# Optimization experiments

Hardware: AMD Instinct MI355X
Metric: run time of the kernel (lower is better)

The kernel has to match this reference:

```python
import jax, jax.numpy as jnp
import numpy as np

BN_EPS = 1e-5


def setup_inputs() -> dict:
    key = jax.random.key(0)
    ks = jax.random.split(key, 8)
    B, N, D = 16, 16384, 64
    NP, NS = 1024, 32
    inp = {
        "xyz": jax.random.normal(ks[0], (B, 3, N), dtype=jnp.float32),
        "points": jax.random.normal(ks[1], (B, D, N), dtype=jnp.float32),
        "fps_init": jax.random.randint(ks[2], (B,), 0, N, dtype=jnp.int32),
        "group_idx": jax.random.randint(ks[3], (B, NP, NS), 0, N, dtype=jnp.int32),
    }
    chans = [67, 64, 128, 128]
    for i in range(3):
        cin, cout = chans[i], chans[i + 1]
        wk = jax.random.fold_in(ks[4], i)
        inp[f"W{i}"] = jax.random.normal(wk, (cout, cin), dtype=jnp.float32) * (1.0 / np.sqrt(cin))
        inp[f"b{i}"] = jnp.zeros((cout,), dtype=jnp.float32)
        inp[f"g{i}"] = jnp.ones((cout,), dtype=jnp.float32)
        inp[f"be{i}"] = jnp.zeros((cout,), dtype=jnp.float32)
    return inp


def _fps(x, init_far, npoint):
    # x: [B,N,3]; iterative furthest point sampling, npoint sequential steps
    B, N, _ = x.shape

    def step(carry, _):
        dist, far = carry
        c = jnp.take_along_axis(x, far[:, None, None], axis=1)  # [B,1,3]
        d = jnp.sum((x - c) ** 2, axis=-1)                       # [B,N]
        dist = jnp.minimum(dist, d)
        return (dist, jnp.argmax(dist, axis=-1).astype(far.dtype)), far

    init = (jnp.full((B, N), 1e10, dtype=x.dtype), init_far)
    _, cents = jax.lax.scan(step, init, None, length=npoint)
    return cents.T  # [B, npoint]


def _conv_bn_relu(h, W, b, g, be):
    # h: [B, np, ns, Cin]; 1x1 conv == channel matmul; BN (training stats) over (B,np,ns)
    y = jnp.einsum('bskc,oc->bsko', h, W) + b
    m = y.mean(axis=(0, 1, 2))
    v = y.var(axis=(0, 1, 2))
    y = (y - m) * jax.lax.rsqrt(v + BN_EPS) * g + be
    return jax.nn.relu(y)


def reference(xyz, points, fps_init, group_idx,
              W0, b0, g0, be0, W1, b1, g1, be1, W2, b2, g2, be2):
    x = jnp.transpose(xyz, (0, 2, 1))     # [B,N,3]
    p = jnp.transpose(points, (0, 2, 1))  # [B,N,D]
    B, N, _ = x.shape
    NP, NS = group_idx.shape[1], group_idx.shape[2]

    cents = _fps(x, fps_init, NP)                                   # [B,NP]
    new_xyz = jnp.take_along_axis(x, cents[:, :, None], axis=1)     # [B,NP,3]

    flat = group_idx.reshape(B, NP * NS)
    gx = jnp.take_along_axis(x, flat[:, :, None], axis=1).reshape(B, NP, NS, 3)
    gp = jnp.take_along_axis(p, flat[:, :, None], axis=1).reshape(B, NP, NS, -1)
    h = jnp.concatenate([gx, gp], axis=-1)  # [B,NP,NS,67]

    h = _conv_bn_relu(h, W0, b0, g0, be0)
    h = _conv_bn_relu(h, W1, b1, g1, be1)
    h = _conv_bn_relu(h, W2, b2, g2, be2)
    new_points = h.max(axis=2)              # max over nsample -> [B,NP,Cout]

    return jnp.transpose(new_xyz, (0, 2, 1)), jnp.transpose(new_points, (0, 2, 1))
```

## Files before the change

kernel.cpp:

```cpp
#include <hip/hip_runtime.h>

typedef short bf16x8 __attribute__((ext_vector_type(8)));
typedef float f32x4 __attribute__((ext_vector_type(4)));
typedef float f32x2 __attribute__((ext_vector_type(2)));
typedef unsigned short u16;
typedef unsigned int u32;
typedef unsigned long long u64;

#define NPTS 16384
#define NPOINT 1024
#define STOT 524288
#define NCB 240
#define NW  960

__device__ __forceinline__ u16 f2bf(float f){
  u32 u = __builtin_bit_cast(u32, f);
  u += 0x7fffu + ((u >> 16) & 1u);
  return (u16)(u >> 16);
}
__device__ __forceinline__ float bf2f(u16 u){
  u32 x = ((u32)u) << 16;
  return __builtin_bit_cast(float, x);
}

template<int CTRL>
__device__ __forceinline__ float dpp_maxf(float v){
  int x = __builtin_amdgcn_update_dpp(0, __builtin_bit_cast(int, v), CTRL, 0xf, 0xf, true);
  return fmaxf(v, __builtin_bit_cast(float, x));
}
template<int CTRL>
__device__ __forceinline__ u64 dpp_max(u64 key){
  u32 lo = (u32)key, hi = (u32)(key >> 32);
  u32 lo1 = (u32)__builtin_amdgcn_update_dpp(0, (int)lo, CTRL, 0xf, 0xf, true);
  u32 hi1 = (u32)__builtin_amdgcn_update_dpp(0, (int)hi, CTRL, 0xf, 0xf, true);
  u64 k1 = ((u64)hi1 << 32) | (u64)lo1;
  return (k1 > key) ? k1 : key;
}
__device__ __forceinline__ u64 packkey(float d, int idx){
  return ((u64)__builtin_bit_cast(u32, d) << 32) | (u64)(u32)(~(u32)idx);
}

__device__ __forceinline__ void arrive(u32* c){
  __hip_atomic_fetch_add(c, 1u, __ATOMIC_RELEASE, __HIP_MEMORY_SCOPE_AGENT);
}
__device__ __forceinline__ void waitc(u32* c, u32 tgt){
  while (__hip_atomic_load(c, __ATOMIC_ACQUIRE, __HIP_MEMORY_SCOPE_AGENT) < tgt)
    __builtin_amdgcn_s_sleep(16);
}

struct FpsS  { uint2 wkey[2][16]; float4 csl[2]; };
struct ConvS { float lsum[128]; float lsqr[128]; float av[128]; float dv[128]; };
union SMemU  { FpsS fps; ConvS conv; };

__device__ __forceinline__ bf16x8 load_bn_relu(const u16* __restrict__ row, int ko,
                                               const float* __restrict__ av,
                                               const float* __restrict__ dv){
  uint4 r = *(const uint4*)(row + ko);
  u32 w[4] = {r.x, r.y, r.z, r.w};
  bf16x8 out;
#pragma unroll
  for (int jj = 0; jj < 8; jj++){
    u16 us = (u16)(w[jj >> 1] >> ((jj & 1) * 16));
    float h = fmaxf(fmaf(av[ko + jj], bf2f(us), dv[ko + jj]), 0.f);
    out[jj] = (short)f2bf(h);
  }
  return out;
}

__global__ void zero_kernel(u32* __restrict__ ctrs){
  if (threadIdx.x < 64) ctrs[threadIdx.x] = 0;
}

__global__ __launch_bounds__(1024, 4) void mega_kernel(
    const float* __restrict__ xyz, const float* __restrict__ points,
    const int* __restrict__ finit, const int* __restrict__ gidx,
    const float* __restrict__ W0, const float* __restrict__ g0v, const float* __restrict__ be0,
    const float* __restrict__ W1, const float* __restrict__ g1v, const float* __restrict__ be1,
    const float* __restrict__ W2, const float* __restrict__ g2v, const float* __restrict__ be2,
    float* __restrict__ out0, float* __restrict__ out1,
    u16* __restrict__ XP, u16* __restrict__ y0, u16* __restrict__ y1,
    float* __restrict__ maxb, float* __restrict__ minb,
    float* __restrict__ statsF,
    u16* __restrict__ W0bf, u16* __restrict__ W1bf, u16* __restrict__ W2bf,
    u32* __restrict__ ctrs){
  __shared__ SMemU sm;
  const int t = threadIdx.x;
  const int wave = t >> 6, lane = t & 63;

  if (blockIdx.x < 16){
    const int b = blockIdx.x;
    const float* xb = xyz + (size_t)b * 3 * NPTS;
    f32x2 px[8], py[8], pz[8], dist[8];
#pragma unroll
    for (int j = 0; j < 8; j++){
      f32x2 x, y, z;
#pragma unroll
      for (int h = 0; h < 2; h++){
        int n = ((2*j + h) << 10) + t;
        x[h] = xb[n];
        y[h] = xb[NPTS + n];
        z[h] = xb[2*NPTS + n];
      }
      px[j] = x; py[j] = y; pz[j] = z;
      f32x2 big = {1e10f, 1e10f};
      dist[j] = big;
    }
    const int far0 = finit[b];
    if (t == (far0 & 1023)){
      int kk = far0 >> 10;
      float sx = px[0].x, sy = py[0].x, sz = pz[0].x;
#pragma unroll
      for (int k = 1; k < 16; k++){
        bool e = (kk == k);
        float vx = px[k>>1][k&1], vy = py[k>>1][k&1], vz = pz[k>>1][k&1];
        sx = e ? vx : sx; sy = e ? vy : sy; sz = e ? vz : sz;
      }
      sm.fps.csl[0] = make_float4(sx, sy, sz, 0.f);
    }
    __syncthreads();
    for (int it = 0; it < NPOINT; it++){
      const int p = it & 1;
      float4 cc = sm.fps.csl[p];
      if (t == 0){
        out0[((size_t)b*3 + 0)*NPOINT + it] = cc.x;
        out0[((size_t)b*3 + 1)*NPOINT + it] = cc.y;
        out0[((size_t)b*3 + 2)*NPOINT + it] = cc.z;
      }
      float bv = -1.f; int bk = 0;
      {
#pragma clang fp contract(off)
        f32x2 cx2 = {cc.x, cc.x}, cy2 = {cc.y, cc.y}, cz2 = {cc.z, cc.z};
#pragma unroll
        for (int j = 0; j < 8; j++){
          f32x2 dx = px[j] - cx2;
          f32x2 dy = py[j] - cy2;
          f32x2 dz = pz[j] - cz2;
          f32x2 dd = dx*dx + dy*dy + dz*dz;
          f32x2 dm = __builtin_elementwise_min(dist[j], dd);
          dist[j] = dm;
          bool g0 = dm.x > bv;
          bv = g0 ? dm.x : bv;  bk = g0 ? (2*j)   : bk;
          bool g1 = dm.y > bv;
          bv = g1 ? dm.y : bv;  bk = g1 ? (2*j+1) : bk;
        }
      }
      float m = bv;
      m = dpp_maxf<0xB1>(m);
      m = dpp_maxf<0x4E>(m);
      m = dpp_maxf<0x141>(m);
      m = dpp_maxf<0x140>(m);
      m = dpp_maxf<0x142>(m);
      m = dpp_maxf<0x143>(m);
      float ms = __builtin_bit_cast(float, __builtin_amdgcn_readlane(__builtin_bit_cast(int, m), 63));
      u64 mk = __ballot(bv == ms);
      u32 widx;
      if (__popcll(mk) == 1){
        int L = (int)__builtin_ctzll(mk);
        int kwin = __builtin_amdgcn_readlane(bk, L);
        widx = (u32)((kwin << 10) + (wave << 6) + L);
      } else {
        u64 key = packkey(bv, (bk << 10) + t);
        key = dpp_max<0xB1>(key); key = dpp_max<0x4E>(key);
        key = dpp_max<0x141>(key); key = dpp_max<0x140>(key);
        key = dpp_max<0x142>(key); key = dpp_max<0x143>(key);
        u32 lo = (u32)__builtin_amdgcn_readlane((int)(u32)key, 63);
        widx = ~lo;
      }
      if (lane == 0){
        uint2 wk; wk.x = widx; wk.y = __builtin_bit_cast(u32, ms);
        sm.fps.wkey[p][wave] = wk;
      }
      __syncthreads();
      uint2 wk = sm.fps.wkey[p][lane & 15];
      float wv = __builtin_bit_cast(float, wk.y);
      float g4 = wv;
      g4 = dpp_maxf<0xB1>(g4); g4 = dpp_maxf<0x4E>(g4);
      g4 = dpp_maxf<0x141>(g4); g4 = dpp_maxf<0x140>(g4);
      float gms = __builtin_bit_cast(float, __builtin_amdgcn_readfirstlane(__builtin_bit_cast(int, g4)));
      u64 mk2 = __ballot(wv == gms);
      u32 lo16 = (u32)mk2 & 0xFFFFu;
      int nb;
      if (__popc(lo16) == 1){
        int w = (int)__builtin_ctz(lo16);
        nb = __builtin_amdgcn_readlane((int)wk.x, w);
      } else {
        u64 k2 = ((u64)wk.y << 32) | (u64)(u32)(~wk.x);
        k2 = dpp_max<0xB1>(k2); k2 = dpp_max<0x4E>(k2);
        k2 = dpp_max<0x141>(k2); k2 = dpp_max<0x140>(k2);
        u32 lo = (u32)__builtin_amdgcn_readfirstlane((int)(u32)k2);
        nb = (int)~lo;
      }
      nb = __builtin_amdgcn_readfirstlane(nb);
      if (t == (nb & 1023)){
        int kk = nb >> 10;
        float sx = px[0].x, sy = py[0].x, sz = pz[0].x;
#pragma unroll
        for (int k = 1; k < 16; k++){
          bool e = (kk == k);
          float vx = px[k>>1][k&1], vy = py[k>>1][k&1], vz = pz[k>>1][k&1];
          sx = e ? vx : sx; sy = e ? vy : sy; sz = e ? vz : sz;
        }
        sm.fps.csl[p ^ 1] = make_float4(sx, sy, sz, 0.f);
      }
      __syncthreads();
    }
    return;
  }

  const int cb = blockIdx.x - 16;
  const int lw = wave & 3, g = wave >> 2;
  const int Wk = cb*4 + g;
  const int lrow = lane & 15, lq = lane >> 4;
  float* bsum0 = statsF;          float* bsqr0 = statsF + 8192;
  float* bsum1 = statsF + 16384;  float* bsqr1 = statsF + 24576;
  float* bsum2 = statsF + 32768;  float* bsqr2 = statsF + 40960;
  float* a0 = statsF + 49152;       float* d0 = a0 + 128;
  float* a1 = statsF + 49152 + 256; float* d1 = a1 + 128;
  float* a2 = statsF + 49152 + 512; float* d2 = a2 + 128;

  for (u32 idx = (u32)cb*1024u + t; idx < 16u*16384u; idx += (u32)NCB*1024u){
    u32 b = idx >> 14, n = idx & 16383u;
    const float* xb = xyz + (size_t)b*3*NPTS + n;
    const float* pb = points + (size_t)b*64*NPTS + n;
    u16* dst = XP + ((size_t)b*NPTS + n)*96;
#pragma unroll
    for (int half = 0; half < 2; half++){
      u32 w[24];
#pragma unroll
      for (int q = 0; q < 24; q++){
        int c0 = half*48 + 2*q, c1 = c0 + 1;
        float f0 = (c0 < 3) ? xb[(size_t)c0*NPTS] : (c0 < 67) ? pb[(size_t)(c0-3)*NPTS] : 0.f;
        float f1 = (c1 < 3) ? xb[(size_t)c1*NPTS] : (c1 < 67) ? pb[(size_t)(c1-3)*NPTS] : 0.f;
        w[q] = (u32)f2bf(f0) | ((u32)f2bf(f1) << 16);
      }
#pragma unroll
      for (int q = 0; q < 6; q++){
        uint4 v; v.x = w[4*q]; v.y = w[4*q+1]; v.z = w[4*q+2]; v.w = w[4*q+3];
        *(uint4*)(dst + half*48 + q*8) = v;
      }
    }
  }
  if (cb == 0){
    for (int i = t; i < 64*96; i += 1024){
      int nn = i / 96, kk = i % 96;
      W0bf[i] = (kk < 67) ? f2bf(W0[nn*67 + kk]) : (u16)0;
    }
    for (int i = t; i < 128*64; i += 1024) W1bf[i] = f2bf(W1[i]);
    for (int i = t; i < 128*128; i += 1024) W2bf[i] = f2bf(W2[i]);
  }
  if (cb == 1){
    for (int i = t; i < 49152; i += 1024) statsF[i] = 0.f;
  }
  __threadfence();
  __syncthreads();
  if (t == 0){ arrive(&ctrs[0]); waitc(&ctrs[0], NCB); }
  __syncthreads();

  if (t < 128){ sm.conv.lsum[t] = 0.f; sm.conv.lsqr[t] = 0.f; }
  __syncthreads();
  for (int j2 = Wk; j2 < 4096; j2 += NW){
    const int b = j2 >> 8;
    const size_t srow = (size_t)j2 * 128;
    const int gbase = b*32768 + (j2 & 255)*128;
    const int m0 = lw*32 + lrow, m1 = m0 + 16;
    const int p0 = gidx[gbase + m0];
    const int p1 = gidx[gbase + m1];
    const bf16x8* ar0 = (const bf16x8*)(XP + ((size_t)b*NPTS + p0)*96);
    const bf16x8* ar1 = (const bf16x8*)(XP + ((size_t)b*NPTS + p1)*96);
    f32x4 acc[2][4];
#pragma unroll
    for (int mt = 0; mt < 2; mt++)
#pragma unroll
      for (int nt = 0; nt < 4; nt++){ f32x4 z = {0.f,0.f,0.f,0.f}; acc[mt][nt] = z; }
#pragma unroll
    for (int ks = 0; ks < 3; ks++){
      bf16x8 af0 = ar0[ks*4 + lq];
      bf16x8 af1 = ar1[ks*4 + lq];
#pragma unroll
      for (int nt = 0; nt < 4; nt++){
        bf16x8 bb = *(const bf16x8*)(W0bf + (nt*16 + lrow)*96 + ks*32 + lq*8);
        acc[0][nt] = __builtin_amdgcn_mfma_f32_16x16x32_bf16(af0, bb, acc[0][nt], 0, 0, 0);
        acc[1][nt] = __builtin_amdgcn_mfma_f32_16x16x32_bf16(af1, bb, acc[1][nt], 0, 0, 0);
      }
    }
#pragma unroll
    for (int nt = 0; nt < 4; nt++){
      float s = 0.f, s2 = 0.f;
#pragma unroll
      for (int mt = 0; mt < 2; mt++){
#pragma unroll
        for (int i = 0; i < 4; i++){
          float u = acc[mt][nt][i];
          s += u; s2 = fmaf(u, u, s2);
          int m = lw*32 + mt*16 + lq*4 + i;
          y0[(srow + m)*64 + nt*16 + lrow] = f2bf(u);
        }
      }
      s  += __shfl_xor(s, 16, 64);  s  += __shfl_xor(s, 32, 64);
      s2 += __shfl_xor(s2, 16, 64); s2 += __shfl_xor(s2, 32, 64);
      if (lane < 16){ atomicAdd(&sm.conv.lsum[nt*16 + lane], s); atomicAdd(&sm.conv.lsqr[nt*16 + lane], s2); }
    }
  }
  __syncthreads();
  if (t < 64){
    atomicAdd(&bsum0[(cb & 63)*128 + t], sm.conv.lsum[t]);
    atomicAdd(&bsqr0[(cb & 63)*128 + t], sm.conv.lsqr[t]);
  }
  __threadfence();
  __syncthreads();
  if (t == 0) arrive(&ctrs[1]);
  if (cb == 0){
    if (t == 0) waitc(&ctrs[1], NCB);
    __syncthreads();
    if (t < 64){
      float s = 0.f, s2 = 0.f;
      for (int k = 0; k < 64; k++){ s += bsum0[k*128 + t]; s2 += bsqr0[k*128 + t]; }
      const float inv = 1.f / (float)STOT;
      float m = s * inv, v = s2 * inv - m*m;
      float aa = g0v[t] / sqrtf(v + 1e-5f);
      a0[t] = aa; d0[t] = be0[t] - m*aa;
    }
    __threadfence();
    __syncthreads();
    if (t == 0) arrive(&ctrs[2]);
  }
  if (t == 0) waitc(&ctrs[2], 1);
  __syncthreads();

  if (t < 128){ sm.conv.lsum[t] = 0.f; sm.conv.lsqr[t] = 0.f; }
  if (t < 64){ sm.conv.av[t] = a0[t]; sm.conv.dv[t] = d0[t]; }
  __syncthreads();
  for (int j2 = Wk; j2 < 4096; j2 += NW){
    const size_t srow = (size_t)j2 * 128;
    const int m0 = lw*32 + lrow, m1 = m0 + 16;
    const u16* row0 = y0 + (srow + m0)*64;
    const u16* row1 = y0 + (srow + m1)*64;
    f32x4 acc[2][8];
#pragma unroll
    for (int mt = 0; mt < 2; mt++)
#pragma unroll
      for (int nt = 0; nt < 8; nt++){ f32x4 z = {0.f,0.f,0.f,0.f}; acc[mt][nt] = z; }
#pragma unroll
    for (int ks = 0; ks < 2; ks++){
      const int ko = ks*32 + lq*8;
      bf16x8 af0 = load_bn_relu(row0, ko, sm.conv.av, sm.conv.dv);
      bf16x8 af1 = load_bn_relu(row1, ko, sm.conv.av, sm.conv.dv);
#pragma unroll
      for (int nt = 0; nt < 8; nt++){
        bf16x8 bb = *(const bf16x8*)(W1bf + (nt*16 + lrow)*64 + ko);
        acc[0][nt] = __builtin_amdgcn_mfma_f32_16x16x32_bf16(af0, bb, acc[0][nt], 0, 0, 0);
        acc[1][nt] = __builtin_amdgcn_mfma_f32_16x16x32_bf16(af1, bb, acc[1][nt], 0, 0, 0);
      }
    }
#pragma unroll
    for (int nt = 0; nt < 8; nt++){
      float s = 0.f, s2 = 0.f;
#pragma unroll
      for (int mt = 0; mt < 2; mt++){
#pragma unroll
        for (int i = 0; i < 4; i++){
          float u = acc[mt][nt][i];
          s += u; s2 = fmaf(u, u, s2);
          int m = lw*32 + mt*16 + lq*4 + i;
          y1[(srow + m)*128 + nt*16 + lrow] = f2bf(u);
        }
      }
      s  += __shfl_xor(s, 16, 64);  s  += __shfl_xor(s, 32, 64);
      s2 += __shfl_xor(s2, 16, 64); s2 += __shfl_xor(s2, 32, 64);
      if (lane < 16){ atomicAdd(&sm.conv.lsum[nt*16 + lane], s); atomicAdd(&sm.conv.lsqr[nt*16 + lane], s2); }
    }
  }
  __syncthreads();
  if (t < 128){
    atomicAdd(&bsum1[(cb & 63)*128 + t], sm.conv.lsum[t]);
    atomicAdd(&bsqr1[(cb & 63)*128 + t], sm.conv.lsqr[t]);
  }
  __threadfence();
  __syncthreads();
  if (t == 0) arrive(&ctrs[3]);
  if (cb == 0){
    if (t == 0) waitc(&ctrs[3], NCB);
    __syncthreads();
    if (t < 128){
      float s = 0.f, s2 = 0.f;
      for (int k = 0; k < 64; k++){ s += bsum1[k*128 + t]; s2 += bsqr1[k*128 + t]; }
      const float inv = 1.f / (float)STOT;
      float m = s * inv, v = s2 * inv - m*m;
      float aa = g1v[t] / sqrtf(v + 1e-5f);
      a1[t] = aa; d1[t] = be1[t] - m*aa;
    }
    __threadfence();
    __syncthreads();
    if (t == 0) arrive(&ctrs[4]);
  }
  if (t == 0) waitc(&ctrs[4], 1);
  __syncthreads();

  if (t < 128){ sm.conv.lsum[t] = 0.f; sm.conv.lsqr[t] = 0.f;
                sm.conv.av[t] = a1[t]; sm.conv.dv[t] = d1[t]; }
  __syncthreads();
  for (int j2 = Wk; j2 < 4096; j2 += NW){
    const size_t srow = (size_t)j2 * 128;
    const int m0 = lw*32 + lrow, m1 = m0 + 16;
    const u16* row0 = y1 + (srow + m0)*128;
    const u16* row1 = y1 + (srow + m1)*128;
    f32x4 acc[2][8];
#pragma unroll
    for (int mt = 0; mt < 2; mt++)
#pragma unroll
      for (int nt = 0; nt < 8; nt++){ f32x4 z = {0.f,0.f,0.f,0.f}; acc[mt][nt] = z; }
#pragma unroll
    for (int ks = 0; ks < 4; ks++){
      const int ko = ks*32 + lq*8;
      bf16x8 af0 = load_bn_relu(row0, ko, sm.conv.av, sm.conv.dv);
      bf16x8 af1 = load_bn_relu(row1, ko, sm.conv.av, sm.conv.dv);
#pragma unroll
      for (int nt = 0; nt < 8; nt++){
        bf16x8 bb = *(const bf16x8*)(W2bf + (nt*16 + lrow)*128 + ko);
        acc[0][nt] = __builtin_amdgcn_mfma_f32_16x16x32_bf16(af0, bb, acc[0][nt], 0, 0, 0);
        acc[1][nt] = __builtin_amdgcn_mfma_f32_16x16x32_bf16(af1, bb, acc[1][nt], 0, 0, 0);
      }
    }
#pragma unroll
    for (int nt = 0; nt < 8; nt++){
      float s = 0.f, s2 = 0.f, mx = -3.4e38f, mn = 3.4e38f;
#pragma unroll
      for (int mt = 0; mt < 2; mt++){
#pragma unroll
        for (int i = 0; i < 4; i++){
          float u = acc[mt][nt][i];
          s += u; s2 = fmaf(u, u, s2);
          mx = fmaxf(mx, u); mn = fminf(mn, u);
        }
      }
      s  += __shfl_xor(s, 16, 64);  s  += __shfl_xor(s, 32, 64);
      s2 += __shfl_xor(s2, 16, 64); s2 += __shfl_xor(s2, 32, 64);
      mx = fmaxf(mx, __shfl_xor(mx, 16, 64)); mx = fmaxf(mx, __shfl_xor(mx, 32, 64));
      mn = fminf(mn, __shfl_xor(mn, 16, 64)); mn = fminf(mn, __shfl_xor(mn, 32, 64));
      if (lane < 16){
        size_t gi = ((size_t)j2*4 + lw)*128 + nt*16 + lane;
        maxb[gi] = mx; minb[gi] = mn;
        atomicAdd(&sm.conv.lsum[nt*16 + lane], s); atomicAdd(&sm.conv.lsqr[nt*16 + lane], s2);
      }
    }
  }
  __syncthreads();
  if (t < 128){
    atomicAdd(&bsum2[(cb & 63)*128 + t], sm.conv.lsum[t]);
    atomicAdd(&bsqr2[(cb & 63)*128 + t], sm.conv.lsqr[t]);
  }
  __threadfence();
  __syncthreads();
  if (t == 0) arrive(&ctrs[5]);
  if (cb == 0){
    if (t == 0) waitc(&ctrs[5], NCB);
    __syncthreads();
    if (t < 128){
      float s = 0.f, s2 = 0.f;
      for (int k = 0; k < 64; k++){ s += bsum2[k*128 + t]; s2 += bsqr2[k*128 + t]; }
      const float inv = 1.f / (float)STOT;
      float m = s * inv, v = s2 * inv - m*m;
      float aa = g2v[t] / sqrtf(v + 1e-5f);
      a2[t] = aa; d2[t] = be2[t] - m*aa;
    }
    __threadfence();
    __syncthreads();
    if (t == 0) arrive(&ctrs[6]);
  }
  if (t == 0) waitc(&ctrs[6], 1);
  __syncthreads();

  for (u32 e = (u32)cb*1024u + t; e < 16u*1024u*128u; e += (u32)NCB*1024u){
    u32 np = e & 1023u;
    u32 c  = (e >> 10) & 127u;
    u32 b  = e >> 17;
    size_t gi = ((size_t)b*1024 + np)*128 + c;
    float a = a2[c];
    float v = (a >= 0.f) ? maxb[gi] : minb[gi];
    out1[((size_t)b*128 + c)*1024 + np] = fmaxf(fmaf(a, v, d2[c]), 0.f);
  }
}

extern "C" void kernel_launch(void* const* d_in, const int* in_sizes, int n_in,
                              void* d_out, int out_size, void* d_ws, size_t ws_size,
                              hipStream_t stream) {
  const float* xyz    = (const float*)d_in[0];
  const float* points = (const float*)d_in[1];
  const int*   finit  = (const int*)d_in[2];
  const int*   gidx   = (const int*)d_in[3];
  const float* W0  = (const float*)d_in[4];
  const float* g0v = (const float*)d_in[6];
  const float* be0 = (const float*)d_in[7];
  const float* W1  = (const float*)d_in[8];
  const float* g1v = (const float*)d_in[10];
  const float* be1 = (const float*)d_in[11];
  const float* W2  = (const float*)d_in[12];
  const float* g2v = (const float*)d_in[14];
  const float* be2 = (const float*)d_in[15];

  float* out0 = (float*)d_out;
  float* out1 = out0 + 16*3*NPOINT;

  char* ws = (char*)d_ws;
  u16* y1 = (u16*)ws;
  u16* XP = (u16*)ws;
  u16* y0 = (u16*)(ws + 134217728);
  float* maxb = (float*)(ws + 134217728);
  float* minb = (float*)(ws + 134217728 + 8388608);
  float* statsF = (float*)(ws + 201326592);
  u16* W0bf = (u16*)(ws + 201326592 + 49920*4);
  u16* W1bf = W0bf + 64*96;
  u16* W2bf = W1bf + 128*64;
  u32* ctrs = (u32*)(ws + 205782016);

  zero_kernel<<<1, 64, 0, stream>>>(ctrs);
  mega_kernel<<<256, 1024, 0, stream>>>(
      xyz, points, finit, gidx,
      W0, g0v, be0, W1, g1v, be1, W2, g2v, be2,
      out0, out1, XP, y0, y1, maxb, minb, statsF,
      W0bf, W1bf, W2bf, ctrs);
}
```

Measured before the change: 1.911 ms.

## Split each batch's FPS across four blocks with global-memory argmax exchange

Furthest point sampling for each batch was done by one 1024-thread block. It is now split across four blocks of 256 active threads, each owning 4096 points. Every iteration, each block publishes its local winner key and coordinates to global slots, bumps an atomic counter, and spins until all four have arrived, then reduces the four keys to get the next centroid. This shortens the in-block reduction and spreads the sequential FPS work over more CUs, but adds a cross-block global atomic handshake on every one of the 1024 iterations. It also leaves fewer blocks for the convolution phase.

```diff
diff --git a/kernel.cpp b/kernel.cpp
--- a/kernel.cpp
+++ b/kernel.cpp
@@ -10,8 +10,9 @@
 #define NPTS 16384
 #define NPOINT 1024
 #define STOT 524288
-#define NCB 240
-#define NW  960
+#define NFB 64
+#define NCB 192
+#define NW  768
 
 __device__ __forceinline__ u16 f2bf(float f){
   u32 u = __builtin_bit_cast(u32, f);
@@ -47,10 +48,16 @@
   while (__hip_atomic_load(c, __ATOMIC_ACQUIRE, __HIP_MEMORY_SCOPE_AGENT) < tgt)
     __builtin_amdgcn_s_sleep(16);
 }
-
-struct FpsS  { uint2 wkey[2][16]; float4 csl[2]; };
+__device__ __forceinline__ void waitf(u32* c, u32 tgt){
+  while (__hip_atomic_load(c, __ATOMIC_ACQUIRE, __HIP_MEMORY_SCOPE_AGENT) < tgt)
+    __builtin_amdgcn_s_sleep(1);
+}
+
+struct FpsS  { uint2 wkey[2][4]; float4 csl[2]; };
 struct ConvS { float lsum[128]; float lsqr[128]; float av[128]; float dv[128]; };
 union SMemU  { FpsS fps; ConvS conv; };
+
+struct FSlot { uint4 a; u32 khi; u32 pad3[3]; };
 
 __device__ __forceinline__ bf16x8 load_bn_relu(const u16* __restrict__ row, int ko,
                                                const float* __restrict__ av,
@@ -82,13 +89,19 @@
     float* __restrict__ maxb, float* __restrict__ minb,
     float* __restrict__ statsF,
     u16* __restrict__ W0bf, u16* __restrict__ W1bf, u16* __restrict__ W2bf,
+    FSlot* __restrict__ fslot, float4* __restrict__ isl,
     u32* __restrict__ ctrs){
   __shared__ SMemU sm;
   const int t = threadIdx.x;
   const int wave = t >> 6, lane = t & 63;
 
-  if (blockIdx.x < 16){
-    const int b = blockIdx.x;
+  if (blockIdx.x < NFB){
+    const int b  = blockIdx.x & 15;
+    const int sb = blockIdx.x >> 4;
+    if (t >= 256) return;
+    const int wv4 = t >> 6;
+    u32* ctr = &ctrs[32 + b];
+    FSlot* sl = fslot + b * 8;
     const float* xb = xyz + (size_t)b * 3 * NPTS;
     f32x2 px[8], py[8], pz[8], dist[8];
 #pragma unroll
@@ -96,7 +109,7 @@
       f32x2 x, y, z;
 #pragma unroll
       for (int h = 0; h < 2; h++){
-        int n = ((2*j + h) << 10) + t;
+        int n = (sb << 12) + ((2*j + h) << 8) + t;
         x[h] = xb[n];
         y[h] = xb[NPTS + n];
         z[h] = xb[2*NPTS + n];
@@ -106,8 +119,8 @@
       dist[j] = big;
     }
     const int far0 = finit[b];
-    if (t == (far0 & 1023)){
-      int kk = far0 >> 10;
+    if ((far0 >> 12) == sb && t == (far0 & 255)){
+      int kk = (far0 >> 8) & 15;
       float sx = px[0].x, sy = py[0].x, sz = pz[0].x;
 #pragma unroll
       for (int k = 1; k < 16; k++){
@@ -115,13 +128,19 @@
         float vx = px[k>>1][k&1], vy = py[k>>1][k&1], vz = pz[k>>1][k&1];
         sx = e ? vx : sx; sy = e ? vy : sy; sz = e ? vz : sz;
       }
-      sm.fps.csl[0] = make_float4(sx, sy, sz, 0.f);
+      isl[b] = make_float4(sx, sy, sz, 0.f);
+      __threadfence();
+      __hip_atomic_fetch_add(ctr, 4u, __ATOMIC_RELEASE, __HIP_MEMORY_SCOPE_AGENT);
+    }
+    if (t == 0){
+      waitf(ctr, 4u);
+      sm.fps.csl[0] = isl[b];
     }
     __syncthreads();
     for (int it = 0; it < NPOINT; it++){
       const int p = it & 1;
       float4 cc = sm.fps.csl[p];
-      if (t == 0){
+      if (sb == 0 && t == 0){
         out0[((size_t)b*3 + 0)*NPOINT + it] = cc.x;
         out0[((size_t)b*3 + 1)*NPOINT + it] = cc.y;
         out0[((size_t)b*3 + 2)*NPOINT + it] = cc.z;
@@ -157,9 +176,9 @@
       if (__popcll(mk) == 1){
         int L = (int)__builtin_ctzll(mk);
         int kwin = __builtin_amdgcn_readlane(bk, L);
-        widx = (u32)((kwin << 10) + (wave << 6) + L);
+        widx = (u32)((kwin << 8) + (wv4 << 6) + L);
       } else {
-        u64 key = packkey(bv, (bk << 10) + t);
+        u64 key = packkey(bv, (bk << 8) + t);
         key = dpp_max<0xB1>(key); key = dpp_max<0x4E>(key);
         key = dpp_max<0x141>(key); key = dpp_max<0x140>(key);
         key = dpp_max<0x142>(key); key = dpp_max<0x143>(key);
@@ -168,46 +187,73 @@
       }
       if (lane == 0){
         uint2 wk; wk.x = widx; wk.y = __builtin_bit_cast(u32, ms);
-        sm.fps.wkey[p][wave] = wk;
+        sm.fps.wkey[p][wv4] = wk;
       }
       __syncthreads();
-      uint2 wk = sm.fps.wkey[p][lane & 15];
-      float wv = __builtin_bit_cast(float, wk.y);
-      float g4 = wv;
+      uint2 wk = sm.fps.wkey[p][lane & 3];
+      float wvv = __builtin_bit_cast(float, wk.y);
+      float g4 = wvv;
       g4 = dpp_maxf<0xB1>(g4); g4 = dpp_maxf<0x4E>(g4);
-      g4 = dpp_maxf<0x141>(g4); g4 = dpp_maxf<0x140>(g4);
       float gms = __builtin_bit_cast(float, __builtin_amdgcn_readfirstlane(__builtin_bit_cast(int, g4)));
-      u64 mk2 = __ballot(wv == gms);
-      u32 lo16 = (u32)mk2 & 0xFFFFu;
+      u64 mk2 = __ballot(wvv == gms);
+      u32 lo4 = (u32)mk2 & 0xFu;
       int nb;
-      if (__popc(lo16) == 1){
-        int w = (int)__builtin_ctz(lo16);
+      if (__popc(lo4) == 1){
+        int w = (int)__builtin_ctz(lo4);
         nb = __builtin_amdgcn_readlane((int)wk.x, w);
       } else {
         u64 k2 = ((u64)wk.y << 32) | (u64)(u32)(~wk.x);
         k2 = dpp_max<0xB1>(k2); k2 = dpp_max<0x4E>(k2);
-        k2 = dpp_max<0x141>(k2); k2 = dpp_max<0x140>(k2);
         u32 lo = (u32)__builtin_amdgcn_readfirstlane((int)(u32)k2);
         nb = (int)~lo;
       }
       nb = __builtin_amdgcn_readfirstlane(nb);
-      if (t == (nb & 1023)){
-        int kk = nb >> 10;
-        float sx = px[0].x, sy = py[0].x, sz = pz[0].x;
-#pragma unroll
-        for (int k = 1; k < 16; k++){
-          bool e = (kk == k);
-          float vx = px[k>>1][k&1], vy = py[k>>1][k&1], vz = pz[k>>1][k&1];
-          sx = e ? vx : sx; sy = e ? vy : sy; sz = e ? vz : sz;
+      if (it < NPOINT - 1){
+        if (t == (nb & 255)){
+          int kk = nb >> 8;
+          float sx = px[0].x, sy = py[0].x, sz = pz[0].x;
+#pragma unroll
+          for (int k = 1; k < 16; k++){
+            bool e = (kk == k);
+            float vx = px[k>>1][k&1], vy = py[k>>1][k&1], vz = pz[k>>1][k&1];
+            sx = e ? vx : sx; sy = e ? vy : sy; sz = e ? vz : sz;
+          }
+          u32 gn = (u32)((sb << 12) + nb);
+          FSlot* s = &sl[p*4 + sb];
+          uint4 A;
+          A.x = __builtin_bit_cast(u32, sx);
+          A.y = __builtin_bit_cast(u32, sy);
+          A.z = __builtin_bit_cast(u32, sz);
+          A.w = ~gn;
+          s->a = A;
+          s->khi = __builtin_bit_cast(u32, gms);
+          __threadfence();
+          arrive(ctr);
         }
-        sm.fps.csl[p ^ 1] = make_float4(sx, sy, sz, 0.f);
+        if (t == 0){
+          waitf(ctr, 4u * (u32)(it + 2));
+          u64 bkey = 0; float bx = 0.f, by = 0.f, bz = 0.f;
+#pragma unroll
+          for (int s2 = 0; s2 < 4; s2++){
+            const FSlot* q = &sl[p*4 + s2];
+            uint4 A = q->a; u32 kh = q->khi;
+            u64 key = ((u64)kh << 32) | (u64)A.w;
+            if (key > bkey){
+              bkey = key;
+              bx = __builtin_bit_cast(float, A.x);
+              by = __builtin_bit_cast(float, A.y);
+              bz = __builtin_bit_cast(float, A.z);
+            }
+          }
+          sm.fps.csl[p ^ 1] = make_float4(bx, by, bz, 0.f);
+        }
       }
       __syncthreads();
     }
     return;
   }
 
-  const int cb = blockIdx.x - 16;
+  const int cb = blockIdx.x - NFB;
   const int lw = wave & 3, g = wave >> 2;
   const int Wk = cb*4 + g;
   const int lrow = lane & 15, lq = lane >> 4;
@@ -512,11 +558,13 @@
   u16* W1bf = W0bf + 64*96;
   u16* W2bf = W1bf + 128*64;
   u32* ctrs = (u32*)(ws + 205782016);
+  FSlot* fslot = (FSlot*)(ws + 205782272);
+  float4* isl  = (float4*)(ws + 205786368);
 
   zero_kernel<<<1, 64, 0, stream>>>(ctrs);
   mega_kernel<<<256, 1024, 0, stream>>>(
       xyz, points, finit, gidx,
       W0, g0v, be0, W1, g1v, be1, W2, g2v, be2,
       out0, out1, XP, y0, y1, maxb, minb, statsF,
-      W0bf, W1bf, W2bf, ctrs);
-}
+      W0bf, W1bf, W2bf, fslot, isl, ctrs);
+}
```

Measured after the change: 6.917 ms. 3.62x slower.
